# Performance work log

Hardware: AMD Instinct MI355X
Metric: run time of the kernel (lower is better)

Reference implementation:

```python
import jax, jax.numpy as jnp
import numpy as np

B, S, D, H = 2, 2048, 512, 8
HD = D // H
EPS = 1e-8
SCALE = HD ** -0.5


def setup_inputs() -> dict:
    key = jax.random.key(0)
    ks = jax.random.split(key, 12)
    gene_emb = jax.random.normal(ks[0], (B, S, D), jnp.float32)
    expr_emb = jax.random.normal(ks[1], (B, S, D), jnp.float32)
    M = jax.random.randint(ks[2], (B, S, S), 0, 2).astype(jnp.float32)
    def lin(k, fan_in, fan_out):
        kw, kb = jax.random.split(k)
        bound = 1.0 / np.sqrt(fan_in)
        W = jax.random.uniform(kw, (fan_in, fan_out), jnp.float32, -bound, bound)
        b = jax.random.uniform(kb, (fan_out,), jnp.float32, -bound, bound)
        return W, b
    Wf, bf = lin(ks[3], 2 * D, D)  # fused_emb_proj
    Wq, bq = lin(ks[4], D, D)
    Wk, bk = lin(ks[5], D, D)
    Wv, bv = lin(ks[6], D, D)
    Wo, bo = lin(ks[7], D, D)
    return {"gene_emb": gene_emb, "expr_emb": expr_emb, "M": M,
            "Wf": Wf, "bf": bf, "Wq": Wq, "bq": bq, "Wk": Wk, "bk": bk,
            "Wv": Wv, "bv": bv, "Wo": Wo, "bo": bo}


def reference(gene_emb, expr_emb, M, Wf, bf, Wq, bq, Wk, bk, Wv, bv, Wo, bo):
    # fused=True, self_attention=False path: Q and K from projected concat
    fused = jnp.concatenate([gene_emb, expr_emb], axis=-1) @ Wf + bf  # [B,S,D]
    Q = (fused @ Wq + bq).reshape(B, S, H, HD)
    K = (fused @ Wk + bk).reshape(B, S, H, HD)
    V = (expr_emb @ Wv + bv).reshape(B, S, H, HD)
    scores = jnp.einsum('bqhd,bkhd->bhqk', Q, K) * SCALE  # [B,H,S,S]
    Mh = M[:, None, :, :]  # broadcast over heads
    scores = scores + jnp.where(Mh == 0, -1e9, 0.0)
    attn = jax.nn.softmax(scores, axis=-1)
    A = attn * Mh  # gated weights
    A = A / (jnp.sum(jnp.abs(A), axis=-1, keepdims=True) + EPS)  # abs-sum renorm
    out = jnp.einsum('bhqk,bkhd->bqhd', A, V).reshape(B, S, D)
    return out @ Wo + bo
```

## Files before the change

### kernel.cpp

```cpp
#include <hip/hip_runtime.h>
#include <stdint.h>
#include <math.h>

#define BB 2
#define SS 2048
#define DDIM 512
#define HH 8
#define HDD 64

typedef unsigned short u16;
typedef unsigned int u32;
typedef unsigned long long u64;
typedef short bf16x8 __attribute__((ext_vector_type(8)));
typedef float f32x4 __attribute__((ext_vector_type(4)));

__device__ __forceinline__ u16 f2bf(float x) {
  unsigned int u = __float_as_uint(x);
  unsigned int r = (u + 0x7fffu + ((u >> 16) & 1u)) >> 16;
  return (u16)r;
}

__device__ __forceinline__ u32 cvtpk(float a, float b) {
  u32 r;
  asm("v_cvt_pk_bf16_f32 %0, %1, %2" : "=v"(r) : "v"(a), "v"(b));
  return r;
}

__device__ __forceinline__ void cp16(const void* g, void* l) {
  __builtin_amdgcn_global_load_lds(
      (const __attribute__((address_space(1))) void*)g,
      (__attribute__((address_space(3))) void*)l, 16, 0, 0);
}

__global__ __launch_bounds__(256) void cast_bf16_k(
    const float* __restrict__ g, const float* __restrict__ e,
    u16* __restrict__ og, u16* __restrict__ oe) {
  int i = blockIdx.x * 256 + threadIdx.x;
  float4 a = ((const float4*)g)[i];
  float4 b = ((const float4*)e)[i];
  ushort4 ua, ub;
  ua.x = f2bf(a.x); ua.y = f2bf(a.y); ua.z = f2bf(a.z); ua.w = f2bf(a.w);
  ub.x = f2bf(b.x); ub.y = f2bf(b.y); ub.z = f2bf(b.z); ub.w = f2bf(b.w);
  ((ushort4*)og)[i] = ua;
  ((ushort4*)oe)[i] = ub;
}

__global__ __launch_bounds__(256) void wprep_k(
    const float* __restrict__ Wf, const float* __restrict__ Wq,
    const float* __restrict__ Wk, const float* __restrict__ Wv,
    const float* __restrict__ Wo,
    u16* __restrict__ WfT, u16* __restrict__ WqT, u16* __restrict__ WkT,
    u16* __restrict__ WvT, u16* __restrict__ WoT) {
  int z = blockIdx.z;
  const float* W; u16* WT; int K;
  switch (z) {
    case 0: W = Wf; WT = WfT; K = 1024; break;
    case 1: W = Wq; WT = WqT; K = 512; break;
    case 2: W = Wk; WT = WkT; K = 512; break;
    case 3: W = Wv; WT = WvT; K = 512; break;
    default: W = Wo; WT = WoT; K = 512; break;
  }
  int k0 = blockIdx.y * 32;
  if (k0 >= K) return;
  int n0 = blockIdx.x * 32;
  __shared__ float t[32][33];
  int tx = threadIdx.x & 31, ty = threadIdx.x >> 5;
#pragma unroll
  for (int i = 0; i < 32; i += 8)
    t[ty + i][tx] = W[(size_t)(k0 + ty + i) * DDIM + n0 + tx];
  __syncthreads();
#pragma unroll
  for (int i = 0; i < 32; i += 8)
    WT[(size_t)(n0 + ty + i) * K + k0 + tx] = f2bf(t[tx][ty + i]);
}

__global__ __launch_bounds__(256) void mpack2_k(const float* __restrict__ M,
                                                u64* __restrict__ Mp) {
  int wid = (blockIdx.x * 256 + threadIdx.x) >> 6;
  int lane = threadIdx.x & 63;
#pragma unroll 4
  for (int i = 0; i < 16; ++i) {
    int idx = wid * 16 + i;
    int row = idx >> 3, k = idx & 7;
    float4 v = *(const float4*)&M[(size_t)row * SS + k * 256 + lane * 4];
    u64 b0 = __ballot(v.x != 0.0f);
    u64 b1 = __ballot(v.y != 0.0f);
    u64 b2 = __ballot(v.z != 0.0f);
    u64 b3 = __ballot(v.w != 0.0f);
    if (lane == 0) {
      u64* p = Mp + ((size_t)row * 32 + k * 4);
      p[0] = b0; p[1] = b1; p[2] = b2; p[3] = b3;
    }
  }
}

template <int EPI>
__global__ __launch_bounds__(256) void gemm2_k(
    const u16* __restrict__ A0, const u16* __restrict__ A1,
    const u16* __restrict__ Bt0, const u16* __restrict__ Bt1,
    const u16* __restrict__ Bt2,
    const float* __restrict__ bias0, const float* __restrict__ bias1,
    const float* __restrict__ bias2,
    u16* __restrict__ O0, u16* __restrict__ O1, u16* __restrict__ O2,
    float* __restrict__ OF) {
  constexpr int KSZ = (EPI == 0) ? 1024 : 512;
  constexpr int NIT = KSZ / 64;
  __shared__ alignas(16) u16 Al[2][64 * 64];
  __shared__ alignas(16) u16 Bl[2][64 * 64];

  const int tid = threadIdx.x;
  const int l = tid & 63, w = tid >> 6, lg = l >> 4, lr = l & 15;
  const int wm = w >> 1, wn = w & 1;
  const int m0 = blockIdx.y * 64;
  const int n0 = blockIdx.x * 64;

  const u16* Aa = A0; const u16* Bt = Bt0; const float* bias = bias0;
  int z = 0;
  if (EPI == 1) {
    z = blockIdx.z;
    Aa = (z == 2) ? A1 : A0;
    Bt = (z == 0) ? Bt0 : (z == 1) ? Bt1 : Bt2;
    bias = (z == 0) ? bias0 : (z == 1) ? bias1 : bias2;
  }

  f32x4 zero4 = {0.f, 0.f, 0.f, 0.f};
  f32x4 acc[2][2];
#pragma unroll
  for (int i = 0; i < 2; ++i)
#pragma unroll
    for (int j = 0; j < 2; ++j) acc[i][j] = zero4;

  const int srow = tid >> 3, spos = tid & 7;
  const int sk8 = spos ^ (srow & 7);
  const size_t sdst = (size_t)tid * 16;

  int aOff[2][2], bOff[2][2];
#pragma unroll
  for (int i = 0; i < 2; ++i) {
    int row = 32 * wm + 16 * i + lr;
    aOff[i][0] = row * 128 + ((lg ^ (row & 7)) * 16);
    aOff[i][1] = row * 128 + (((4 + lg) ^ (row & 7)) * 16);
  }
#pragma unroll
  for (int j = 0; j < 2; ++j) {
    int row = 32 * wn + 16 * j + lr;
    bOff[j][0] = row * 128 + ((lg ^ (row & 7)) * 16);
    bOff[j][1] = row * 128 + (((4 + lg) ^ (row & 7)) * 16);
  }

  auto STAGE = [&](int buf, int kt) {
    int kbase = kt * 64 + 8 * sk8;
    const u16* sA;
    if (EPI == 0) {
      const u16* Asrc = (kt < 8) ? A0 : A1;
      int kk = (kt < 8) ? kbase : kbase - 512;
      sA = Asrc + (size_t)(m0 + srow) * 512 + kk;
    } else {
      sA = Aa + (size_t)(m0 + srow) * 512 + kbase;
    }
    const u16* sB = Bt + (size_t)(n0 + srow) * KSZ + kbase;
    cp16(sA, (char*)Al[buf] + sdst);
    cp16(sA + 32 * 512, (char*)Al[buf] + sdst + 4096);
    cp16(sB, (char*)Bl[buf] + sdst);
    cp16(sB + 32 * KSZ, (char*)Bl[buf] + sdst + 4096);
  };

  STAGE(0, 0);
  asm volatile("s_waitcnt vmcnt(0)" ::: "memory");
  __syncthreads();

  int cur = 0;
  for (int kt = 0; kt < NIT; ++kt) {
    if (kt + 1 < NIT) STAGE(cur ^ 1, kt + 1);
    const char* Ab = (const char*)Al[cur];
    const char* Bb = (const char*)Bl[cur];
    bf16x8 af[2][2], bfr[2][2];
#pragma unroll
    for (int i = 0; i < 2; ++i) {
      af[i][0] = *(const bf16x8*)(Ab + aOff[i][0]);
      af[i][1] = *(const bf16x8*)(Ab + aOff[i][1]);
    }
#pragma unroll
    for (int j = 0; j < 2; ++j) {
      bfr[j][0] = *(const bf16x8*)(Bb + bOff[j][0]);
      bfr[j][1] = *(const bf16x8*)(Bb + bOff[j][1]);
    }
#pragma unroll
    for (int kk = 0; kk < 2; ++kk)
#pragma unroll
      for (int i = 0; i < 2; ++i)
#pragma unroll
        for (int j = 0; j < 2; ++j)
          acc[i][j] = __builtin_amdgcn_mfma_f32_16x16x32_bf16(
              af[i][kk], bfr[j][kk], acc[i][j], 0, 0, 0);
    asm volatile("s_waitcnt vmcnt(0)" ::: "memory");
    __syncthreads();
    cur ^= 1;
  }

#pragma unroll
  for (int j = 0; j < 2; ++j) {
    int c = n0 + 32 * wn + 16 * j + lr;
    float bv = bias[c];
#pragma unroll
    for (int i = 0; i < 2; ++i) {
      int qb = m0 + 32 * wm + 16 * i + 4 * lg;
      if (EPI == 0) {
#pragma unroll
        for (int r = 0; r < 4; ++r)
          O0[(size_t)(qb + r) * 512 + c] = f2bf(acc[i][j][r] + bv);
      } else if (EPI == 2) {
#pragma unroll
        for (int r = 0; r < 4; ++r)
          OF[(size_t)(qb + r) * 512 + c] = acc[i][j][r] + bv;
      } else {
        int b = qb >> 11, s = qb & 2047;
        int hh = c >> 6, hd = c & 63;
        if (z < 2) {
          const float qsc = (z == 0) ? 0.18033688011112042f : 1.0f;
          u16* O = (z == 0) ? O0 : O1;
#pragma unroll
          for (int r = 0; r < 4; ++r)
            O[((size_t)(b * HH + hh) * SS + s + r) * HDD + hd] =
                f2bf((acc[i][j][r] + bv) * qsc);
        } else {
          ushort4 v;
          v.x = f2bf(acc[i][j][0] + bv);
          v.y = f2bf(acc[i][j][1] + bv);
          v.z = f2bf(acc[i][j][2] + bv);
          v.w = f2bf(acc[i][j][3] + bv);
          *(ushort4*)(O2 + ((size_t)(b * HH + hh) * HDD + hd) * SS + s) = v;
        }
      }
    }
  }
}

__global__ __launch_bounds__(256) void attn5_k(
    const u16* __restrict__ Qh, const u16* __restrict__ Kh,
    const u16* __restrict__ Vt, const u64* __restrict__ Mp,
    u16* __restrict__ AO) {
  __shared__ alignas(16) u16 Kl[2][64 * 64];
  __shared__ alignas(16) u16 Vl[2][64 * 64];
  __shared__ alignas(16) u16 Pl[4][16 * 64];

  const int tid = threadIdx.x;
  const int l = tid & 63, w = tid >> 6, lg = l >> 4, lr = l & 15;
  const int bh = blockIdx.y, b = bh >> 3, h = bh & 7;
  const int qw = blockIdx.x * 64 + 16 * w;

  bf16x8 qf0, qf1;
  {
    const u16* qp = Qh + ((size_t)bh * SS + qw + lr) * HDD + 8 * lg;
    qf0 = *(const bf16x8*)qp;
    qf1 = *(const bf16x8*)(qp + 32);
  }

  f32x4 zero4 = {0.f, 0.f, 0.f, 0.f};
  f32x4 o[4];
#pragma unroll
  for (int t4 = 0; t4 < 4; ++t4) o[t4] = zero4;
  float mrun = -INFINITY, lrun = 0.f;

  const u64* Mrow = Mp + ((size_t)b * SS + qw + lr) * 32;
  u64 mp[4], mpN[4];
#pragma unroll
  for (int r = 0; r < 4; ++r) mp[r] = Mrow[r];

  int kOff[4][2], vOff[4][2], pOff[2], wOff[4];
#pragma unroll
  for (int g = 0; g < 4; ++g) {
    int krow = 16 * g + lr;
    kOff[g][0] = krow * 128 + ((lg ^ (krow & 7)) * 16);
    kOff[g][1] = krow * 128 + (((4 + lg) ^ (krow & 7)) * 16);
  }
#pragma unroll
  for (int t4 = 0; t4 < 4; ++t4) {
    int vrow = 16 * t4 + lr;
    vOff[t4][0] = vrow * 128 + ((lg ^ (vrow & 7)) * 16);
    vOff[t4][1] = vrow * 128 + (((4 + lg) ^ (vrow & 7)) * 16);
  }
#pragma unroll
  for (int kk = 0; kk < 2; ++kk)
    pOff[kk] = lr * 128 + (((4 * kk + lg) ^ (lr & 7)) * 16);
#pragma unroll
  for (int g = 0; g < 4; ++g)
    wOff[g] = lr * 128 + (((2 * g + (lg >> 1)) ^ (lr & 7)) * 16) + (lg & 1) * 8;

  const int srow = tid >> 3, spos = tid & 7;
  const int sk8 = spos ^ (srow & 7);
  const size_t sdst = (size_t)tid * 16;
  const u16* pK0 = Kh + ((size_t)bh * SS + srow) * HDD + 8 * sk8;
  const u16* pK1 = pK0 + 32 * HDD;
  const u16* pV0 = Vt + ((size_t)bh * HDD + srow) * SS + 8 * sk8;
  const u16* pV1 = pV0 + 32 * SS;

  cp16(pK0, (char*)Kl[0] + sdst);
  cp16(pK1, (char*)Kl[0] + sdst + 4096);
  cp16(pV0, (char*)Vl[0] + sdst);
  cp16(pV1, (char*)Vl[0] + sdst + 4096);
  asm volatile("s_waitcnt vmcnt(0)" ::: "memory");
  __syncthreads();

  u16* Pw = Pl[w];
  int cur = 0;
  for (int kt = 0; kt < 32; ++kt) {
    if (kt < 31) {
      pK0 += 64 * HDD; pK1 += 64 * HDD; pV0 += 64; pV1 += 64;
      char* kd = (char*)Kl[cur ^ 1];
      char* vd = (char*)Vl[cur ^ 1];
      cp16(pK0, kd + sdst);
      cp16(pK1, kd + sdst + 4096);
      cp16(pV0, vd + sdst);
      cp16(pV1, vd + sdst + 4096);
    }
    const int tm = kt & 3;
    if (tm == 0 && kt < 28) {
#pragma unroll
      for (int r = 0; r < 4; ++r) mpN[r] = Mrow[((kt >> 2) + 1) * 4 + r];
    }

    const char* Klw = (const char*)Kl[cur];
    const char* Vlw = (const char*)Vl[cur];

    f32x4 sc[4];
#pragma unroll
    for (int g = 0; g < 4; ++g) {
      bf16x8 k0f = *(const bf16x8*)(Klw + kOff[g][0]);
      bf16x8 k1f = *(const bf16x8*)(Klw + kOff[g][1]);
      f32x4 zz = zero4;
      zz = __builtin_amdgcn_mfma_f32_16x16x32_bf16(k0f, qf0, zz, 0, 0, 0);
      zz = __builtin_amdgcn_mfma_f32_16x16x32_bf16(k1f, qf1, zz, 0, 0, 0);
      sc[g] = zz;
    }
    {
      u32 wb[4];
#pragma unroll
      for (int r = 0; r < 4; ++r) wb[r] = (u32)(mp[r] >> (16 * tm + lg));
#pragma unroll
      for (int g = 0; g < 4; ++g)
#pragma unroll
        for (int r = 0; r < 4; ++r)
          if (!((wb[r] >> (4 * g)) & 1u)) sc[g][r] = -INFINITY;
    }
    float t = sc[0][0];
#pragma unroll
    for (int g = 0; g < 4; ++g)
#pragma unroll
      for (int r = 0; r < 4; ++r) t = fmaxf(t, sc[g][r]);
    t = fmaxf(t, __shfl_xor(t, 16));
    t = fmaxf(t, __shfl_xor(t, 32));
    float mnew = fmaxf(mrun, t);
    float fac = (mnew == -INFINITY) ? 1.0f : exp2f(mrun - mnew);
    float msafe = fmaxf(mnew, -1e30f);
    float psum = 0.f;
#pragma unroll
    for (int g = 0; g < 4; ++g)
#pragma unroll
      for (int r = 0; r < 4; ++r) {
        float p = exp2f(sc[g][r] - msafe);
        sc[g][r] = p;
        psum += p;
      }
    psum += __shfl_xor(psum, 16);
    psum += __shfl_xor(psum, 32);
    mrun = mnew;
    lrun = lrun * fac + psum;
#pragma unroll
    for (int t4 = 0; t4 < 4; ++t4) o[t4] *= fac;
#pragma unroll
    for (int g = 0; g < 4; ++g) {
      uint2 pv;
      pv.x = cvtpk(sc[g][0], sc[g][1]);
      pv.y = cvtpk(sc[g][2], sc[g][3]);
      *(uint2*)((char*)Pw + wOff[g]) = pv;
    }
#pragma unroll
    for (int kk = 0; kk < 2; ++kk) {
      bf16x8 pf = *(const bf16x8*)((const char*)Pw + pOff[kk]);
#pragma unroll
      for (int t4 = 0; t4 < 4; ++t4) {
        bf16x8 vf = *(const bf16x8*)(Vlw + vOff[t4][kk]);
        o[t4] = __builtin_amdgcn_mfma_f32_16x16x32_bf16(vf, pf, o[t4], 0, 0, 0);
      }
    }
    if (tm == 3) {
#pragma unroll
      for (int r = 0; r < 4; ++r) mp[r] = mpN[r];
    }
    asm volatile("s_waitcnt vmcnt(0)" ::: "memory");
    __syncthreads();
    cur ^= 1;
  }

  float inv = (lrun > 0.f) ? 1.0f / (lrun + 1e-8f) : 0.f;
  u16* op = AO + ((size_t)b * SS + qw + lr) * DDIM + h * HDD + 4 * lg;
#pragma unroll
  for (int t4 = 0; t4 < 4; ++t4) {
    ushort4 v;
    v.x = f2bf(o[t4][0] * inv);
    v.y = f2bf(o[t4][1] * inv);
    v.z = f2bf(o[t4][2] * inv);
    v.w = f2bf(o[t4][3] * inv);
    *(ushort4*)(op + 16 * t4) = v;
  }
}

extern "C" void kernel_launch(void* const* d_in, const int* in_sizes, int n_in,
                              void* d_out, int out_size, void* d_ws, size_t ws_size,
                              hipStream_t stream) {
  if (ws_size < (size_t)(31.5 * 1024 * 1024)) return;

  const float* gene = (const float*)d_in[0];
  const float* expr = (const float*)d_in[1];
  const float* Mm = (const float*)d_in[2];
  const float* Wf = (const float*)d_in[3];
  const float* bf = (const float*)d_in[4];
  const float* Wq = (const float*)d_in[5];
  const float* bq = (const float*)d_in[6];
  const float* Wk = (const float*)d_in[7];
  const float* bk = (const float*)d_in[8];
  const float* Wv = (const float*)d_in[9];
  const float* bv = (const float*)d_in[10];
  const float* Wo = (const float*)d_in[11];
  const float* bo = (const float*)d_in[12];
  float* out = (float*)d_out;

  char* ws = (char*)d_ws;
  const size_t MB4 = 4194304;
  u16* geneB = (u16*)(ws + 0 * MB4);
  u16* exprB = (u16*)(ws + 1 * MB4);
  u16* fusedB = (u16*)(ws + 2 * MB4);
  u16* QhB = (u16*)(ws + 3 * MB4);
  u16* KhB = (u16*)(ws + 4 * MB4);
  u16* VtB = (u16*)(ws + 5 * MB4);
  u16* attnB = (u16*)(ws + 6 * MB4);
  u16* WfT = (u16*)(ws + 7 * MB4);
  u16* WqT = (u16*)(ws + 7 * MB4 + 1048576);
  u16* WkT = (u16*)(ws + 7 * MB4 + 1048576 + 524288);
  u16* WvT = (u16*)(ws + 7 * MB4 + 1048576 + 2 * 524288);
  u16* WoT = (u16*)(ws + 7 * MB4 + 1048576 + 3 * 524288);
  u64* MpB = (u64*)(ws + 0 * MB4);

  cast_bf16_k<<<2048, 256, 0, stream>>>(gene, expr, geneB, exprB);
  wprep_k<<<dim3(16, 32, 5), 256, 0, stream>>>(Wf, Wq, Wk, Wv, Wo, WfT, WqT,
                                               WkT, WvT, WoT);
  gemm2_k<0><<<dim3(8, 64), 256, 0, stream>>>(geneB, exprB, WfT, nullptr, nullptr,
                                              bf, nullptr, nullptr, fusedB,
                                              nullptr, nullptr, nullptr);
  mpack2_k<<<512, 256, 0, stream>>>(Mm, MpB);
  gemm2_k<1><<<dim3(8, 64, 3), 256, 0, stream>>>(fusedB, exprB, WqT, WkT, WvT,
                                                 bq, bk, bv, QhB, KhB, VtB,
                                                 nullptr);
  attn5_k<<<dim3(32, 16), 256, 0, stream>>>(QhB, KhB, VtB, MpB, attnB);
  gemm2_k<2><<<dim3(8, 64), 256, 0, stream>>>(attnB, nullptr, WoT, nullptr,
                                              nullptr, bo, nullptr, nullptr,
                                              nullptr, nullptr, nullptr, out);
}
```

Before: 225.6 us.

## Split attention keys across two wave groups and merge launches

The attention kernel now uses 512 threads per block, where two groups of four waves each process half of the key range with their own double-buffered K/V tiles. The partial softmax states are merged through shared memory at the end. Separately, the bf16 cast and weight transpose kernels are fused into one launch, and the mask bit-packing is folded into the QKV GEMM launch as extra blocks. This cuts kernel launch count and doubles the parallel work per attention block, at the cost of more shared memory, a final merge step, and possibly lower occupancy.

```diff
diff --git a/kernel.cpp b/kernel.cpp
--- a/kernel.cpp
+++ b/kernel.cpp
@@ -32,38 +32,40 @@
       (__attribute__((address_space(3))) void*)l, 16, 0, 0);
 }
 
-__global__ __launch_bounds__(256) void cast_bf16_k(
-    const float* __restrict__ g, const float* __restrict__ e,
-    u16* __restrict__ og, u16* __restrict__ oe) {
-  int i = blockIdx.x * 256 + threadIdx.x;
-  float4 a = ((const float4*)g)[i];
-  float4 b = ((const float4*)e)[i];
-  ushort4 ua, ub;
-  ua.x = f2bf(a.x); ua.y = f2bf(a.y); ua.z = f2bf(a.z); ua.w = f2bf(a.w);
-  ub.x = f2bf(b.x); ub.y = f2bf(b.y); ub.z = f2bf(b.z); ub.w = f2bf(b.w);
-  ((ushort4*)og)[i] = ua;
-  ((ushort4*)oe)[i] = ub;
-}
-
-__global__ __launch_bounds__(256) void wprep_k(
+__global__ __launch_bounds__(256) void prep_k(
+    const float* __restrict__ gene, const float* __restrict__ expr,
     const float* __restrict__ Wf, const float* __restrict__ Wq,
     const float* __restrict__ Wk, const float* __restrict__ Wv,
     const float* __restrict__ Wo,
+    u16* __restrict__ og, u16* __restrict__ oe,
     u16* __restrict__ WfT, u16* __restrict__ WqT, u16* __restrict__ WkT,
     u16* __restrict__ WvT, u16* __restrict__ WoT) {
-  int z = blockIdx.z;
+  __shared__ float t[32][33];
+  const int bid = blockIdx.x;
+  if (bid < 2048) {
+    int i = bid * 256 + threadIdx.x;
+    float4 a = ((const float4*)gene)[i];
+    float4 b = ((const float4*)expr)[i];
+    ushort4 ua, ub;
+    ua.x = f2bf(a.x); ua.y = f2bf(a.y); ua.z = f2bf(a.z); ua.w = f2bf(a.w);
+    ub.x = f2bf(b.x); ub.y = f2bf(b.y); ub.z = f2bf(b.z); ub.w = f2bf(b.w);
+    ((ushort4*)og)[i] = ua;
+    ((ushort4*)oe)[i] = ub;
+    return;
+  }
+  int bi = bid - 2048;
+  int bx = bi & 15, by = (bi >> 4) & 31, bz = bi >> 9;
   const float* W; u16* WT; int K;
-  switch (z) {
+  switch (bz) {
     case 0: W = Wf; WT = WfT; K = 1024; break;
     case 1: W = Wq; WT = WqT; K = 512; break;
     case 2: W = Wk; WT = WkT; K = 512; break;
     case 3: W = Wv; WT = WvT; K = 512; break;
     default: W = Wo; WT = WoT; K = 512; break;
   }
-  int k0 = blockIdx.y * 32;
+  int k0 = by * 32;
   if (k0 >= K) return;
-  int n0 = blockIdx.x * 32;
-  __shared__ float t[32][33];
+  int n0 = bx * 32;
   int tx = threadIdx.x & 31, ty = threadIdx.x >> 5;
 #pragma unroll
   for (int i = 0; i < 32; i += 8)
@@ -74,35 +76,11 @@
     WT[(size_t)(n0 + ty + i) * K + k0 + tx] = f2bf(t[tx][ty + i]);
 }
 
-__global__ __launch_bounds__(256) void mpack2_k(const float* __restrict__ M,
-                                                u64* __restrict__ Mp) {
-  int wid = (blockIdx.x * 256 + threadIdx.x) >> 6;
-  int lane = threadIdx.x & 63;
-#pragma unroll 4
-  for (int i = 0; i < 16; ++i) {
-    int idx = wid * 16 + i;
-    int row = idx >> 3, k = idx & 7;
-    float4 v = *(const float4*)&M[(size_t)row * SS + k * 256 + lane * 4];
-    u64 b0 = __ballot(v.x != 0.0f);
-    u64 b1 = __ballot(v.y != 0.0f);
-    u64 b2 = __ballot(v.z != 0.0f);
-    u64 b3 = __ballot(v.w != 0.0f);
-    if (lane == 0) {
-      u64* p = Mp + ((size_t)row * 32 + k * 4);
-      p[0] = b0; p[1] = b1; p[2] = b2; p[3] = b3;
-    }
-  }
-}
-
 template <int EPI>
 __global__ __launch_bounds__(256) void gemm2_k(
     const u16* __restrict__ A0, const u16* __restrict__ A1,
-    const u16* __restrict__ Bt0, const u16* __restrict__ Bt1,
-    const u16* __restrict__ Bt2,
-    const float* __restrict__ bias0, const float* __restrict__ bias1,
-    const float* __restrict__ bias2,
-    u16* __restrict__ O0, u16* __restrict__ O1, u16* __restrict__ O2,
-    float* __restrict__ OF) {
+    const u16* __restrict__ Bt0, const float* __restrict__ bias0,
+    u16* __restrict__ O0, float* __restrict__ OF) {
   constexpr int KSZ = (EPI == 0) ? 1024 : 512;
   constexpr int NIT = KSZ / 64;
   __shared__ alignas(16) u16 Al[2][64 * 64];
@@ -113,15 +91,6 @@
   const int wm = w >> 1, wn = w & 1;
   const int m0 = blockIdx.y * 64;
   const int n0 = blockIdx.x * 64;
-
-  const u16* Aa = A0; const u16* Bt = Bt0; const float* bias = bias0;
-  int z = 0;
-  if (EPI == 1) {
-    z = blockIdx.z;
-    Aa = (z == 2) ? A1 : A0;
-    Bt = (z == 0) ? Bt0 : (z == 1) ? Bt1 : Bt2;
-    bias = (z == 0) ? bias0 : (z == 1) ? bias1 : bias2;
-  }
 
   f32x4 zero4 = {0.f, 0.f, 0.f, 0.f};
   f32x4 acc[2][2];
@@ -156,9 +125,9 @@
       int kk = (kt < 8) ? kbase : kbase - 512;
       sA = Asrc + (size_t)(m0 + srow) * 512 + kk;
     } else {
-      sA = Aa + (size_t)(m0 + srow) * 512 + kbase;
-    }
-    const u16* sB = Bt + (size_t)(n0 + srow) * KSZ + kbase;
+      sA = A0 + (size_t)(m0 + srow) * 512 + kbase;
+    }
+    const u16* sB = Bt0 + (size_t)(n0 + srow) * KSZ + kbase;
     cp16(sA, (char*)Al[buf] + sdst);
     cp16(sA + 32 * 512, (char*)Al[buf] + sdst + 4096);
     cp16(sB, (char*)Bl[buf] + sdst);
@@ -201,7 +170,7 @@
 #pragma unroll
   for (int j = 0; j < 2; ++j) {
     int c = n0 + 32 * wn + 16 * j + lr;
-    float bv = bias[c];
+    float bv = bias0[c];
 #pragma unroll
     for (int i = 0; i < 2; ++i) {
       int qb = m0 + 32 * wm + 16 * i + 4 * lg;
@@ -209,45 +178,166 @@
 #pragma unroll
         for (int r = 0; r < 4; ++r)
           O0[(size_t)(qb + r) * 512 + c] = f2bf(acc[i][j][r] + bv);
-      } else if (EPI == 2) {
+      } else {
 #pragma unroll
         for (int r = 0; r < 4; ++r)
           OF[(size_t)(qb + r) * 512 + c] = acc[i][j][r] + bv;
+      }
+    }
+  }
+}
+
+__global__ __launch_bounds__(256) void gemmqkv_k(
+    const u16* __restrict__ A0 , const u16* __restrict__ A1 ,
+    const u16* __restrict__ Bt0, const u16* __restrict__ Bt1,
+    const u16* __restrict__ Bt2,
+    const float* __restrict__ bias0, const float* __restrict__ bias1,
+    const float* __restrict__ bias2,
+    u16* __restrict__ O0, u16* __restrict__ O1, u16* __restrict__ O2,
+    const float* __restrict__ Mm, u64* __restrict__ Mp) {
+  __shared__ alignas(16) u16 Al[2][64 * 64];
+  __shared__ alignas(16) u16 Bl[2][64 * 64];
+
+  const int bid = blockIdx.x;
+  const int tid = threadIdx.x;
+  if (bid >= 1536) {
+    int bi = bid - 1536;
+    int wid = (bi * 256 + tid) >> 6;
+    int lane = tid & 63;
+#pragma unroll 4
+    for (int i = 0; i < 16; ++i) {
+      int idx = wid * 16 + i;
+      int row = idx >> 3, k = idx & 7;
+      float4 v = *(const float4*)&Mm[(size_t)row * SS + k * 256 + lane * 4];
+      u64 b0 = __ballot(v.x != 0.0f);
+      u64 b1 = __ballot(v.y != 0.0f);
+      u64 b2 = __ballot(v.z != 0.0f);
+      u64 b3 = __ballot(v.w != 0.0f);
+      if (lane == 0) {
+        u64* p = Mp + ((size_t)row * 32 + k * 4);
+        p[0] = b0; p[1] = b1; p[2] = b2; p[3] = b3;
+      }
+    }
+    return;
+  }
+  const int bx = bid & 7, by = (bid >> 3) & 63, bz = bid >> 9;
+  const int l = tid & 63, w = tid >> 6, lg = l >> 4, lr = l & 15;
+  const int wm = w >> 1, wn = w & 1;
+  const int m0 = by * 64, n0 = bx * 64;
+
+  const u16* Aa = (bz == 2) ? A1 : A0;
+  const u16* Bt = (bz == 0) ? Bt0 : (bz == 1) ? Bt1 : Bt2;
+  const float* bias = (bz == 0) ? bias0 : (bz == 1) ? bias1 : bias2;
+
+  f32x4 zero4 = {0.f, 0.f, 0.f, 0.f};
+  f32x4 acc[2][2];
+#pragma unroll
+  for (int i = 0; i < 2; ++i)
+#pragma unroll
+    for (int j = 0; j < 2; ++j) acc[i][j] = zero4;
+
+  const int srow = tid >> 3, spos = tid & 7;
+  const int sk8 = spos ^ (srow & 7);
+  const size_t sdst = (size_t)tid * 16;
+
+  int aOff[2][2], bOff[2][2];
+#pragma unroll
+  for (int i = 0; i < 2; ++i) {
+    int row = 32 * wm + 16 * i + lr;
+    aOff[i][0] = row * 128 + ((lg ^ (row & 7)) * 16);
+    aOff[i][1] = row * 128 + (((4 + lg) ^ (row & 7)) * 16);
+  }
+#pragma unroll
+  for (int j = 0; j < 2; ++j) {
+    int row = 32 * wn + 16 * j + lr;
+    bOff[j][0] = row * 128 + ((lg ^ (row & 7)) * 16);
+    bOff[j][1] = row * 128 + (((4 + lg) ^ (row & 7)) * 16);
+  }
+
+  auto STAGE = [&](int buf, int kt) {
+    int kbase = kt * 64 + 8 * sk8;
+    const u16* sA = Aa + (size_t)(m0 + srow) * 512 + kbase;
+    const u16* sB = Bt + (size_t)(n0 + srow) * 512 + kbase;
+    cp16(sA, (char*)Al[buf] + sdst);
+    cp16(sA + 32 * 512, (char*)Al[buf] + sdst + 4096);
+    cp16(sB, (char*)Bl[buf] + sdst);
+    cp16(sB + 32 * 512, (char*)Bl[buf] + sdst + 4096);
+  };
+
+  STAGE(0, 0);
+  asm volatile("s_waitcnt vmcnt(0)" ::: "memory");
+  __syncthreads();
+
+  int cur = 0;
+  for (int kt = 0; kt < 8; ++kt) {
+    if (kt + 1 < 8) STAGE(cur ^ 1, kt + 1);
+    const char* Ab = (const char*)Al[cur];
+    const char* Bb = (const char*)Bl[cur];
+    bf16x8 af[2][2], bfr[2][2];
+#pragma unroll
+    for (int i = 0; i < 2; ++i) {
+      af[i][0] = *(const bf16x8*)(Ab + aOff[i][0]);
+      af[i][1] = *(const bf16x8*)(Ab + aOff[i][1]);
+    }
+#pragma unroll
+    for (int j = 0; j < 2; ++j) {
+      bfr[j][0] = *(const bf16x8*)(Bb + bOff[j][0]);
+      bfr[j][1] = *(const bf16x8*)(Bb + bOff[j][1]);
+    }
+#pragma unroll
+    for (int kk = 0; kk < 2; ++kk)
+#pragma unroll
+      for (int i = 0; i < 2; ++i)
+#pragma unroll
+        for (int j = 0; j < 2; ++j)
+          acc[i][j] = __builtin_amdgcn_mfma_f32_16x16x32_bf16(
+              af[i][kk], bfr[j][kk], acc[i][j], 0, 0, 0);
+    asm volatile("s_waitcnt vmcnt(0)" ::: "memory");
+    __syncthreads();
+    cur ^= 1;
+  }
+
+#pragma unroll
+  for (int j = 0; j < 2; ++j) {
+    int c = n0 + 32 * wn + 16 * j + lr;
+    float bv = bias[c];
+#pragma unroll
+    for (int i = 0; i < 2; ++i) {
+      int qb = m0 + 32 * wm + 16 * i + 4 * lg;
+      int b = qb >> 11, s = qb & 2047;
+      int hh = c >> 6, hd = c & 63;
+      if (bz < 2) {
+        const float qsc = (bz == 0) ? 0.18033688011112042f : 1.0f;
+        u16* O = (bz == 0) ? O0 : O1;
+#pragma unroll
+        for (int r = 0; r < 4; ++r)
+          O[((size_t)(b * HH + hh) * SS + s + r) * HDD + hd] =
+              f2bf((acc[i][j][r] + bv) * qsc);
       } else {
-        int b = qb >> 11, s = qb & 2047;
-        int hh = c >> 6, hd = c & 63;
-        if (z < 2) {
-          const float qsc = (z == 0) ? 0.18033688011112042f : 1.0f;
-          u16* O = (z == 0) ? O0 : O1;
-#pragma unroll
-          for (int r = 0; r < 4; ++r)
-            O[((size_t)(b * HH + hh) * SS + s + r) * HDD + hd] =
-                f2bf((acc[i][j][r] + bv) * qsc);
-        } else {
-          ushort4 v;
-          v.x = f2bf(acc[i][j][0] + bv);
-          v.y = f2bf(acc[i][j][1] + bv);
-          v.z = f2bf(acc[i][j][2] + bv);
-          v.w = f2bf(acc[i][j][3] + bv);
-          *(ushort4*)(O2 + ((size_t)(b * HH + hh) * HDD + hd) * SS + s) = v;
-        }
+        ushort4 v;
+        v.x = f2bf(acc[i][j][0] + bv);
+        v.y = f2bf(acc[i][j][1] + bv);
+        v.z = f2bf(acc[i][j][2] + bv);
+        v.w = f2bf(acc[i][j][3] + bv);
+        *(ushort4*)(O2 + ((size_t)(b * HH + hh) * HDD + hd) * SS + s) = v;
       }
     }
   }
 }
 
-__global__ __launch_bounds__(256) void attn5_k(
+__global__ __launch_bounds__(512) void attn6_k(
     const u16* __restrict__ Qh, const u16* __restrict__ Kh,
     const u16* __restrict__ Vt, const u64* __restrict__ Mp,
     u16* __restrict__ AO) {
-  __shared__ alignas(16) u16 Kl[2][64 * 64];
-  __shared__ alignas(16) u16 Vl[2][64 * 64];
-  __shared__ alignas(16) u16 Pl[4][16 * 64];
+  __shared__ alignas(16) u16 Kl[2][2][64 * 64];
+  __shared__ alignas(16) u16 Vl[2][2][64 * 64];
+  __shared__ alignas(16) u16 Pl[8][16 * 64];
 
   const int tid = threadIdx.x;
   const int l = tid & 63, w = tid >> 6, lg = l >> 4, lr = l & 15;
+  const int qg = w & 3, kh = w >> 2;
   const int bh = blockIdx.y, b = bh >> 3, h = bh & 7;
-  const int qw = blockIdx.x * 64 + 16 * w;
+  const int qw = blockIdx.x * 64 + 16 * qg;
 
   bf16x8 qf0, qf1;
   {
@@ -265,7 +355,7 @@
   const u64* Mrow = Mp + ((size_t)b * SS + qw + lr) * 32;
   u64 mp[4], mpN[4];
 #pragma unroll
-  for (int r = 0; r < 4; ++r) mp[r] = Mrow[r];
+  for (int r = 0; r < 4; ++r) mp[r] = Mrow[16 * kh + r];
 
   int kOff[4][2], vOff[4][2], pOff[2], wOff[4];
 #pragma unroll
@@ -290,38 +380,37 @@
   const int srow = tid >> 3, spos = tid & 7;
   const int sk8 = spos ^ (srow & 7);
   const size_t sdst = (size_t)tid * 16;
-  const u16* pK0 = Kh + ((size_t)bh * SS + srow) * HDD + 8 * sk8;
-  const u16* pK1 = pK0 + 32 * HDD;
-  const u16* pV0 = Vt + ((size_t)bh * HDD + srow) * SS + 8 * sk8;
-  const u16* pV1 = pV0 + 32 * SS;
-
-  cp16(pK0, (char*)Kl[0] + sdst);
-  cp16(pK1, (char*)Kl[0] + sdst + 4096);
-  cp16(pV0, (char*)Vl[0] + sdst);
-  cp16(pV1, (char*)Vl[0] + sdst + 4096);
+  const u16* pKa = Kh + ((size_t)bh * SS + srow) * HDD + 8 * sk8;
+  const u16* pKb = pKa + (size_t)1024 * HDD;
+  const u16* pVa = Vt + ((size_t)bh * HDD + srow) * SS + 8 * sk8;
+  const u16* pVb = pVa + 1024;
+
+  cp16(pKa, (char*)Kl[0][0] + sdst);
+  cp16(pKb, (char*)Kl[1][0] + sdst);
+  cp16(pVa, (char*)Vl[0][0] + sdst);
+  cp16(pVb, (char*)Vl[1][0] + sdst);
   asm volatile("s_waitcnt vmcnt(0)" ::: "memory");
   __syncthreads();
 
   u16* Pw = Pl[w];
   int cur = 0;
-  for (int kt = 0; kt < 32; ++kt) {
-    if (kt < 31) {
-      pK0 += 64 * HDD; pK1 += 64 * HDD; pV0 += 64; pV1 += 64;
-      char* kd = (char*)Kl[cur ^ 1];
-      char* vd = (char*)Vl[cur ^ 1];
-      cp16(pK0, kd + sdst);
-      cp16(pK1, kd + sdst + 4096);
-      cp16(pV0, vd + sdst);
-      cp16(pV1, vd + sdst + 4096);
+  for (int kt = 0; kt < 16; ++kt) {
+    if (kt < 15) {
+      pKa += 64 * HDD; pKb += 64 * HDD; pVa += 64; pVb += 64;
+      cp16(pKa, (char*)Kl[0][cur ^ 1] + sdst);
+      cp16(pKb, (char*)Kl[1][cur ^ 1] + sdst);
+      cp16(pVa, (char*)Vl[0][cur ^ 1] + sdst);
+      cp16(pVb, (char*)Vl[1][cur ^ 1] + sdst);
     }
     const int tm = kt & 3;
-    if (tm == 0 && kt < 28) {
-#pragma unroll
-      for (int r = 0; r < 4; ++r) mpN[r] = Mrow[((kt >> 2) + 1) * 4 + r];
-    }
-
-    const char* Klw = (const char*)Kl[cur];
-    const char* Vlw = (const char*)Vl[cur];
+    if (tm == 0 && kt < 12) {
+#pragma unroll
+      for (int r = 0; r < 4; ++r)
+        mpN[r] = Mrow[(4 * kh + (kt >> 2) + 1) * 4 + r];
+    }
+
+    const char* Klw = (const char*)Kl[kh][cur];
+    const char* Vlw = (const char*)Vl[kh][cur];
 
     f32x4 sc[4];
 #pragma unroll
@@ -393,16 +482,34 @@
     cur ^= 1;
   }
 
-  float inv = (lrun > 0.f) ? 1.0f / (lrun + 1e-8f) : 0.f;
-  u16* op = AO + ((size_t)b * SS + qw + lr) * DDIM + h * HDD + 4 * lg;
-#pragma unroll
-  for (int t4 = 0; t4 < 4; ++t4) {
-    ushort4 v;
-    v.x = f2bf(o[t4][0] * inv);
-    v.y = f2bf(o[t4][1] * inv);
-    v.z = f2bf(o[t4][2] * inv);
-    v.w = f2bf(o[t4][3] * inv);
-    *(ushort4*)(op + 16 * t4) = v;
+  float* sh = (float*)&Kl[0][0][0];
+  if (kh == 1) {
+    float* p = sh + (size_t)(qg * 64 + l) * 18;
+    p[0] = mrun; p[1] = lrun;
+#pragma unroll
+    for (int t4 = 0; t4 < 4; ++t4)
+#pragma unroll
+      for (int r = 0; r < 4; ++r) p[2 + 4 * t4 + r] = o[t4][r];
+  }
+  __syncthreads();
+  if (kh == 0) {
+    const float* p = sh + (size_t)(qg * 64 + l) * 18;
+    float mB = p[0], lB = p[1];
+    float ms = fmaxf(mrun, mB);
+    float fa = (mrun == -INFINITY) ? 0.f : exp2f(mrun - ms);
+    float fb = (mB == -INFINITY) ? 0.f : exp2f(mB - ms);
+    float ls = lrun * fa + lB * fb;
+    float inv = (ls > 0.f) ? 1.0f / (ls + 1e-8f) : 0.f;
+    u16* op = AO + ((size_t)b * SS + qw + lr) * DDIM + h * HDD + 4 * lg;
+#pragma unroll
+    for (int t4 = 0; t4 < 4; ++t4) {
+      ushort4 v;
+      v.x = f2bf((o[t4][0] * fa + p[2 + 4 * t4 + 0] * fb) * inv);
+      v.y = f2bf((o[t4][1] * fa + p[2 + 4 * t4 + 1] * fb) * inv);
+      v.z = f2bf((o[t4][2] * fa + p[2 + 4 * t4 + 2] * fb) * inv);
+      v.w = f2bf((o[t4][3] * fa + p[2 + 4 * t4 + 3] * fb) * inv);
+      *(ushort4*)(op + 16 * t4) = v;
+    }
   }
 }
 
@@ -442,18 +549,13 @@
   u16* WoT = (u16*)(ws + 7 * MB4 + 1048576 + 3 * 524288);
   u64* MpB = (u64*)(ws + 0 * MB4);
 
-  cast_bf16_k<<<2048, 256, 0, stream>>>(gene, expr, geneB, exprB);
-  wprep_k<<<dim3(16, 32, 5), 256, 0, stream>>>(Wf, Wq, Wk, Wv, Wo, WfT, WqT,
-                                               WkT, WvT, WoT);
-  gemm2_k<0><<<dim3(8, 64), 256, 0, stream>>>(geneB, exprB, WfT, nullptr, nullptr,
-                                              bf, nullptr, nullptr, fusedB,
-                                              nullptr, nullptr, nullptr);
-  mpack2_k<<<512, 256, 0, stream>>>(Mm, MpB);
-  gemm2_k<1><<<dim3(8, 64, 3), 256, 0, stream>>>(fusedB, exprB, WqT, WkT, WvT,
-                                                 bq, bk, bv, QhB, KhB, VtB,
-                                                 nullptr);
-  attn5_k<<<dim3(32, 16), 256, 0, stream>>>(QhB, KhB, VtB, MpB, attnB);
-  gemm2_k<2><<<dim3(8, 64), 256, 0, stream>>>(attnB, nullptr, WoT, nullptr,
-                                              nullptr, bo, nullptr, nullptr,
-                                              nullptr, nullptr, nullptr, out);
-}
+  prep_k<<<4608, 256, 0, stream>>>(gene, expr, Wf, Wq, Wk, Wv, Wo, geneB, exprB,
+                                   WfT, WqT, WkT, WvT, WoT);
+  gemm2_k<0><<<dim3(8, 64), 256, 0, stream>>>(geneB, exprB, WfT, bf, fusedB,
+                                              nullptr);
+  gemmqkv_k<<<2048, 256, 0, stream>>>(fusedB, exprB, WqT, WkT, WvT, bq, bk, bv,
+                                      QhB, KhB, VtB, Mm, MpB);
+  attn6_k<<<dim3(32, 16), 512, 0, stream>>>(QhB, KhB, VtB, MpB, attnB);
+  gemm2_k<2><<<dim3(8, 64), 256, 0, stream>>>(attnB, nullptr, WoT, bo, nullptr,
+                                              out);
+}
```

Result: faster. 205.9 us (-8.7%).
